# Performance work log

Hardware: AMD Instinct MI355X
Metric: run time of the kernel (lower is better)

Reference implementation:

```python
import jax, jax.numpy as jnp
import numpy as np

EPS = 1e-6

def setup_inputs() -> dict:
    key = jax.random.key(0)
    ks = jax.random.split(key, 7)
    T, B, S, A, D = 512, 32, 64, 8, 32
    x = jax.random.normal(ks[0], (T, B, D), dtype=jnp.float32)
    a = jax.random.normal(ks[1], (T, B, A), dtype=jnp.float32)
    mask = jnp.ones((T, B), dtype=jnp.float32)
    mu = jax.random.normal(ks[2], (S, D), dtype=jnp.float32)
    logv = 0.1 * jax.random.normal(ks[3], (S, D), dtype=jnp.float32)
    init_logits = jax.random.normal(ks[4], (S,), dtype=jnp.float32)
    w_base = 0.1 * jax.random.normal(ks[5], (S, S), dtype=jnp.float32)
    w_act = 0.1 * jax.random.normal(ks[6], (A, S, S), dtype=jnp.float32)
    return {"x": x, "a": a, "mask": mask, "mu": mu, "logv": logv,
            "init_logits": init_logits, "w_base": w_base, "w_act": w_act}

def reference(x, a, mask, mu, logv, init_logits, w_base, w_act):
    T, B, D = x.shape
    S = mu.shape[0]
    # Gaussian (diag) emission log-likelihood for every state: [T, B, S]
    var = jnp.exp(logv)
    diff = x[:, :, None, :] - mu  # [T, B, S, D]
    logp_x = -0.5 * jnp.sum(diff * diff / var + logv + jnp.log(2.0 * jnp.pi), axis=-1)
    # Logistic (action-conditioned) transition matrices for t=1..T-1: [T-1, B, S, S]
    trans = jax.nn.softmax(w_base + jnp.einsum('tba,aij->tbij', a[:-1], w_act), axis=-1)
    logp0 = jax.nn.log_softmax(init_logits)
    # alpha_0
    alpha0 = jax.nn.softmax(logp_x[0] + logp0, axis=-1)

    def fwd_step(b, inp):
        tr, lx = inp
        logp_z = jnp.log(jnp.sum(tr * b[:, :, None] + EPS, axis=-2))
        b_new = jax.nn.softmax(lx + logp_z, axis=-1)
        return b_new, b_new

    _, alpha_rest = jax.lax.scan(fwd_step, alpha0, (trans, logp_x[1:]))
    alpha = jnp.concatenate([alpha0[None], alpha_rest], axis=0)  # [T, B, S]

    log_trans = jnp.log(trans + EPS)

    def bwd_step(logb, inp):
        ltr, lx, m = inp
        new = jax.scipy.special.logsumexp(lx[:, None, :] + ltr + logb[:, None, :], axis=-1)
        new = new * (m[:, None] == 1)
        return new, new

    _, lb = jax.lax.scan(bwd_step, jnp.zeros((B, S), x.dtype),
                         (log_trans, logp_x[1:], mask[1:]), reverse=True)
    log_beta = jnp.concatenate([lb, jnp.zeros((1, B, S), x.dtype)], axis=0)  # [T, B, S]

    # Posterior state marginals
    q_z = jax.nn.softmax(jnp.log(alpha + EPS) + log_beta, axis=-1)
    return q_z
```

## Files before the change

### kernel.cpp

```cpp
#include <hip/hip_runtime.h>
#include <math.h>

#define TT 512
#define BB 32
#define SS 64
#define AA 8
#define DD 32
#define EPSF 1e-6f
#define SEPS (64.0f * 1e-6f)
#define TS 68

__device__ __forceinline__ int   f2i(float x){ return __float_as_int(x); }
__device__ __forceinline__ float i2f(int x){ return __int_as_float(x); }
__device__ __forceinline__ float readlane_f(float v, int l){
  return i2f(__builtin_amdgcn_readlane(f2i(v), l));
}
template<int CTRL, int RMASK>
__device__ __forceinline__ float dpp_add(float x){
  return x + i2f(__builtin_amdgcn_update_dpp(0, f2i(x), CTRL, RMASK, 0xf, true));
}
__device__ __forceinline__ float wave_sum_dpp(float x){
  x = dpp_add<0x111, 0xf>(x);
  x = dpp_add<0x112, 0xf>(x);
  x = dpp_add<0x114, 0xf>(x);
  x = dpp_add<0x118, 0xf>(x);
  x = dpp_add<0x142, 0xa>(x);
  x = dpp_add<0x143, 0xc>(x);
  return readlane_f(x, 63);
}
__device__ __forceinline__ float wave_sum(float v){
  #pragma unroll
  for (int m = 1; m < 64; m <<= 1) v += __shfl_xor(v, m, 64);
  return v;
}
__device__ __forceinline__ float wave_max(float v){
  #pragma unroll
  for (int m = 1; m < 64; m <<= 1) v = fmaxf(v, __shfl_xor(v, m, 64));
  return v;
}
#define BARRIER() asm volatile("s_waitcnt lgkmcnt(0)\n\ts_barrier" ::: "memory")

__global__ void prep_kernel(const float* __restrict__ logv,
                            float* __restrict__ iv, float* __restrict__ cs){
  int gid = blockIdx.x * blockDim.x + threadIdx.x;
  if (gid < SS * DD) iv[gid] = __expf(-logv[gid]);
  if (gid < SS){
    float s = 0.f;
    #pragma unroll
    for (int d = 0; d < DD; ++d) s += logv[gid * DD + d];
    cs[gid] = s + (float)DD * 1.8378770664093453f;
  }
}

__global__ __launch_bounds__(256) void logpx_kernel(
    const float* __restrict__ x, const float* __restrict__ mu,
    const float* __restrict__ iv, const float* __restrict__ cs,
    float* __restrict__ slx_out){
  const int lane = threadIdx.x & 63;
  const int w = threadIdx.x >> 6;
  const int row = blockIdx.x * 4 + w;
  const float* __restrict__ xp  = x  + row * DD;
  const float* __restrict__ mup = mu + lane * DD;
  const float* __restrict__ ivp = iv + lane * DD;
  float acc = 0.f;
  #pragma unroll
  for (int d = 0; d < DD; ++d){
    float diff = xp[d] - mup[d];
    acc = fmaf(diff * diff, ivp[d], acc);
  }
  float lx = -0.5f * (acc + cs[lane]);
  float mx = wave_max(lx);
  slx_out[row * SS + lane] = lx - mx;
}

__global__ __launch_bounds__(768) void scan_kernel(
    const float* __restrict__ slx, const float* __restrict__ mask,
    const float* __restrict__ il, const float* __restrict__ a,
    const float* __restrict__ w_base, const float* __restrict__ w_act,
    float* __restrict__ alpha, float* __restrict__ log_beta){
  const int lane = threadIdx.x & 63;
  const int w    = threadIdx.x >> 6;
  const bool is_fwd = (blockIdx.x < BB);
  const int b = is_fwd ? blockIdx.x : (blockIdx.x - BB);

  __shared__ __align__(16) float tile[3][SS * TS];
  __shared__ float rsp[3][8][SS];
  __shared__ float fpart[2][4][SS];
  __shared__ __align__(16) float aLDS[TT * AA];
  __shared__ float mLDS[TT];

  for (int idx = threadIdx.x; idx < TT * AA; idx += 768){
    int t = idx >> 3, k = idx & 7;
    aLDS[idx] = a[(t * BB + b) * AA + k];
  }
  for (int idx = threadIdx.x; idx < TT; idx += 768)
    mLDS[idx] = mask[idx * BB + b];

  if (w >= 4){
    const int pw = w - 4;
    const int jb = pw * 8;
    float wb[8], wa[8][8];
    #pragma unroll
    for (int jj = 0; jj < 8; ++jj){
      wb[jj] = w_base[lane * SS + jb + jj];
      #pragma unroll
      for (int k = 0; k < 8; ++k)
        wa[k][jj] = w_act[(k * SS + lane) * SS + jb + jj];
    }
    float aa[8], aan[8];
    {
      const int t0 = is_fwd ? 0 : (TT - 2);
      const float* __restrict__ ap = a + (t0 * BB + b) * AA;
      #pragma unroll
      for (int k = 0; k < 8; ++k) aa[k] = ap[k];
      const int t1 = is_fwd ? 1 : (TT - 3);
      const float* __restrict__ ap1 = a + (t1 * BB + b) * AA;
      #pragma unroll
      for (int k = 0; k < 8; ++k) aan[k] = ap1[k];
    }
    {
      float ev[8]; float racc = 0.f;
      #pragma unroll
      for (int jj = 0; jj < 8; ++jj){
        float u = wb[jj];
        #pragma unroll
        for (int k = 0; k < 8; ++k) u = fmaf(aa[k], wa[k][jj], u);
        ev[jj] = __expf(u); racc += ev[jj];
      }
      *(float4*)&tile[0][lane * TS + jb]     = make_float4(ev[0],ev[1],ev[2],ev[3]);
      *(float4*)&tile[0][lane * TS + jb + 4] = make_float4(ev[4],ev[5],ev[6],ev[7]);
      rsp[0][pw][lane] = racc;
    }
    BARRIER();
    int tw = 1;
    for (int s = 0; s < TT - 1; ++s){
      if (s <= TT - 3){
        #pragma unroll
        for (int k = 0; k < 8; ++k) aa[k] = aan[k];
        if (s + 1 <= TT - 3){
          const int tn = is_fwd ? (s + 2) : (TT - 4 - s);
          #pragma unroll
          for (int k = 0; k < 8; ++k) aan[k] = aLDS[tn * AA + k];
        }
        float ev[8]; float racc = 0.f;
        #pragma unroll
        for (int jj = 0; jj < 8; ++jj){
          float u = wb[jj];
          #pragma unroll
          for (int k = 0; k < 8; ++k) u = fmaf(aa[k], wa[k][jj], u);
          ev[jj] = __expf(u); racc += ev[jj];
        }
        *(float4*)&tile[tw][lane * TS + jb]     = make_float4(ev[0],ev[1],ev[2],ev[3]);
        *(float4*)&tile[tw][lane * TS + jb + 4] = make_float4(ev[4],ev[5],ev[6],ev[7]);
        rsp[tw][pw][lane] = racc;
        tw = (tw == 2) ? 0 : tw + 1;
      }
      BARRIER();
    }
  } else if (is_fwd){
    const int wb16 = __builtin_amdgcn_readfirstlane(w * 16);
    float u = __expf(slx[b * SS + lane] + il[lane]);
    float c = __builtin_amdgcn_rcpf(wave_sum_dpp(u));
    if (w == 0) alpha[b * SS + lane] = u * c;
    float slxn = slx[(BB + b) * SS + lane];
    float elxc = 0.f;
    BARRIER();
    int ts = 0;
    for (int s = 0; s < TT - 1; ++s){
      if (s > 0){
        const int fs = (s - 1) & 1;
        float S = (fpart[fs][0][lane] + fpart[fs][1][lane])
                + (fpart[fs][2][lane] + fpart[fs][3][lane]);
        u = elxc * fmaf(c, S, SEPS);
        c = __builtin_amdgcn_rcpf(wave_sum_dpp(u));
        if (w == 0) alpha[(s * BB + b) * SS + lane] = u * c;
      }
      float rs = ((rsp[ts][0][lane] + rsp[ts][1][lane]) + (rsp[ts][2][lane] + rsp[ts][3][lane]))
               + ((rsp[ts][4][lane] + rsp[ts][5][lane]) + (rsp[ts][6][lane] + rsp[ts][7][lane]));
      float va = u * __builtin_amdgcn_rcpf(rs);
      const float* __restrict__ tp = &tile[ts][0];
      float a0 = 0.f, a1 = 0.f, a2 = 0.f, a3 = 0.f;
      #pragma unroll
      for (int r = 0; r < 16; r += 4){
        a0 = fmaf(readlane_f(va, wb16 + r    ), tp[(wb16 + r    ) * TS + lane], a0);
        a1 = fmaf(readlane_f(va, wb16 + r + 1), tp[(wb16 + r + 1) * TS + lane], a1);
        a2 = fmaf(readlane_f(va, wb16 + r + 2), tp[(wb16 + r + 2) * TS + lane], a2);
        a3 = fmaf(readlane_f(va, wb16 + r + 3), tp[(wb16 + r + 3) * TS + lane], a3);
      }
      fpart[s & 1][w][lane] = (a0 + a1) + (a2 + a3);
      elxc = __expf(slxn);
      if (s + 2 <= TT - 1) slxn = slx[((s + 2) * BB + b) * SS + lane];
      ts = (ts == 2) ? 0 : ts + 1;
      BARRIER();
    }
    {
      const int fs = (TT - 2) & 1;
      float S = (fpart[fs][0][lane] + fpart[fs][1][lane])
              + (fpart[fs][2][lane] + fpart[fs][3][lane]);
      u = elxc * fmaf(c, S, SEPS);
      c = __builtin_amdgcn_rcpf(wave_sum_dpp(u));
      if (w == 0) alpha[((TT - 1) * BB + b) * SS + lane] = u * c;
    }
  } else {
    const int wb16 = __builtin_amdgcn_readfirstlane(w * 16);
    float breg = 0.f, rWc = 1.f;
    if (w == 0) log_beta[((TT - 1) * BB + b) * SS + lane] = 0.f;
    float slxc = slx[((TT - 1) * BB + b) * SS + lane];
    float mprev = 1.f;
    BARRIER();
    int ts = 0, pts = 2;
    for (int s = 0; s < TT - 1; ++s){
      if (s > 0){
        const int fs = (s - 1) & 1;
        float eh = (fpart[fs][0][lane] + fpart[fs][1][lane])
                 + (fpart[fs][2][lane] + fpart[fs][3][lane]);
        float rsv = ((rsp[pts][0][lane] + rsp[pts][1][lane]) + (rsp[pts][2][lane] + rsp[pts][3][lane]))
                  + ((rsp[pts][4][lane] + rsp[pts][5][lane]) + (rsp[pts][6][lane] + rsp[pts][7][lane]));
        float v = __logf(fmaf(eh * __builtin_amdgcn_rcpf(rsv), rWc, EPSF));
        breg = (mprev == 1.0f) ? v : 0.0f;
        if (w == 0) log_beta[((TT - 1 - s) * BB + b) * SS + lane] = breg;
      }
      float wgt = __expf(slxc + breg);
      float W = wave_sum_dpp(wgt);
      rWc = __builtin_amdgcn_rcpf(W);
      const float* __restrict__ tp = &tile[ts][lane * TS + wb16];
      float4 e0 = *(const float4*)(tp);
      float4 e1 = *(const float4*)(tp + 4);
      float4 e2 = *(const float4*)(tp + 8);
      float4 e3 = *(const float4*)(tp + 12);
      float a0 = 0.f, a1 = 0.f, a2 = 0.f, a3 = 0.f;
      a0 = fmaf(readlane_f(wgt, wb16 + 0),  e0.x, a0);
      a1 = fmaf(readlane_f(wgt, wb16 + 1),  e0.y, a1);
      a2 = fmaf(readlane_f(wgt, wb16 + 2),  e0.z, a2);
      a3 = fmaf(readlane_f(wgt, wb16 + 3),  e0.w, a3);
      a0 = fmaf(readlane_f(wgt, wb16 + 4),  e1.x, a0);
      a1 = fmaf(readlane_f(wgt, wb16 + 5),  e1.y, a1);
      a2 = fmaf(readlane_f(wgt, wb16 + 6),  e1.z, a2);
      a3 = fmaf(readlane_f(wgt, wb16 + 7),  e1.w, a3);
      a0 = fmaf(readlane_f(wgt, wb16 + 8),  e2.x, a0);
      a1 = fmaf(readlane_f(wgt, wb16 + 9),  e2.y, a1);
      a2 = fmaf(readlane_f(wgt, wb16 + 10), e2.z, a2);
      a3 = fmaf(readlane_f(wgt, wb16 + 11), e2.w, a3);
      a0 = fmaf(readlane_f(wgt, wb16 + 12), e3.x, a0);
      a1 = fmaf(readlane_f(wgt, wb16 + 13), e3.y, a1);
      a2 = fmaf(readlane_f(wgt, wb16 + 14), e3.z, a2);
      a3 = fmaf(readlane_f(wgt, wb16 + 15), e3.w, a3);
      fpart[s & 1][w][lane] = (a0 + a1) + (a2 + a3);
      mprev = mLDS[TT - 1 - s];
      if (s <= TT - 3) slxc = slx[((TT - 2 - s) * BB + b) * SS + lane];
      pts = ts; ts = (ts == 2) ? 0 : ts + 1;
      BARRIER();
    }
    {
      const int fs = (TT - 2) & 1;
      float eh = (fpart[fs][0][lane] + fpart[fs][1][lane])
               + (fpart[fs][2][lane] + fpart[fs][3][lane]);
      float rsv = ((rsp[pts][0][lane] + rsp[pts][1][lane]) + (rsp[pts][2][lane] + rsp[pts][3][lane]))
                + ((rsp[pts][4][lane] + rsp[pts][5][lane]) + (rsp[pts][6][lane] + rsp[pts][7][lane]));
      float v = __logf(fmaf(eh * __builtin_amdgcn_rcpf(rsv), rWc, EPSF));
      breg = (mprev == 1.0f) ? v : 0.0f;
      if (w == 0) log_beta[b * SS + lane] = breg;
    }
  }
}

__global__ __launch_bounds__(256) void qz_kernel(
    const float* __restrict__ alpha, const float* __restrict__ log_beta,
    float* __restrict__ out){
  const int lane = threadIdx.x & 63;
  const int w = threadIdx.x >> 6;
  const int row = blockIdx.x * 4 + w;
  float v = __logf(alpha[row * SS + lane] + EPSF) + log_beta[row * SS + lane];
  float mx = wave_max(v);
  float e = __expf(v - mx);
  float sm = wave_sum(e);
  out[row * SS + lane] = e * __builtin_amdgcn_rcpf(sm);
}

extern "C" void kernel_launch(void* const* d_in, const int* in_sizes, int n_in,
                              void* d_out, int out_size, void* d_ws, size_t ws_size,
                              hipStream_t stream){
  const float* x      = (const float*)d_in[0];
  const float* a      = (const float*)d_in[1];
  const float* mask   = (const float*)d_in[2];
  const float* mu     = (const float*)d_in[3];
  const float* logv   = (const float*)d_in[4];
  const float* il     = (const float*)d_in[5];
  const float* w_base = (const float*)d_in[6];
  const float* w_act  = (const float*)d_in[7];
  float* out = (float*)d_out;

  float* ws = (float*)d_ws;
  const size_t TBS = (size_t)TT * BB * SS;
  float* iv       = ws;
  float* cs       = ws + 2048;
  float* slx      = ws + 4096;
  float* alpha    = slx + TBS;
  float* log_beta = alpha + TBS;

  prep_kernel<<<8, 256, 0, stream>>>(logv, iv, cs);
  logpx_kernel<<<TT * BB / 4, 256, 0, stream>>>(x, mu, iv, cs, slx);
  scan_kernel<<<2 * BB, 768, 0, stream>>>(slx, mask, il, a, w_base, w_act,
                                          alpha, log_beta);
  qz_kernel<<<TT * BB / 4, 256, 0, stream>>>(alpha, log_beta, out);
}
```

Measured before the change: 402.4 us.

## Precompute transition softmax in a parallel kernel and stream it into the scan

Adds a fully parallel kernel that computes all action-conditioned transition softmax matrices and writes them to workspace. A new scan kernel then streams those tiles from global memory into a triple-buffered LDS ring, with prefetch waves, instead of recomputing the softmax inside the serial scan. This removes exp/softmax work from the latency-bound recurrence at the cost of writing and reading about 268 MB of extra memory. The new path runs only when the workspace is large enough, otherwise it falls back to the old kernel.

```diff
diff --git a/kernel.cpp b/kernel.cpp
--- a/kernel.cpp
+++ b/kernel.cpp
@@ -71,6 +71,215 @@
   float lx = -0.5f * (acc + cs[lane]);
   float mx = wave_max(lx);
   slx_out[row * SS + lane] = lx - mx;
+}
+
+__global__ __launch_bounds__(512) void trans_kernel(
+    const float* __restrict__ a, const float* __restrict__ w_base,
+    const float* __restrict__ w_act, float* __restrict__ trans){
+  const int b  = blockIdx.x >> 4;
+  const int tc = blockIdx.x & 15;
+  const int t0 = tc * 32;
+  const int tid = threadIdx.x;
+  const int i  = tid >> 3;
+  const int j0 = (tid & 7) * 8;
+  __shared__ float aS[32 * 8];
+  if (tid < 256)
+    aS[tid] = a[(((t0 + (tid >> 3)) * BB) + b) * AA + (tid & 7)];
+  float wb[8], wa[8][8];
+  #pragma unroll
+  for (int jj = 0; jj < 8; ++jj){
+    wb[jj] = w_base[i * SS + j0 + jj];
+    #pragma unroll
+    for (int k = 0; k < 8; ++k)
+      wa[k][jj] = w_act[(k * SS + i) * SS + j0 + jj];
+  }
+  __syncthreads();
+  const int nt = ((TT - 1) - t0 < 32) ? ((TT - 1) - t0) : 32;
+  for (int tt = 0; tt < nt; ++tt){
+    float aa[8];
+    #pragma unroll
+    for (int k = 0; k < 8; ++k) aa[k] = aS[tt * 8 + k];
+    float ev[8]; float rs = 0.f;
+    #pragma unroll
+    for (int jj = 0; jj < 8; ++jj){
+      float u = wb[jj];
+      #pragma unroll
+      for (int k = 0; k < 8; ++k) u = fmaf(aa[k], wa[k][jj], u);
+      ev[jj] = __expf(u); rs += ev[jj];
+    }
+    rs += __shfl_xor(rs, 1, 64);
+    rs += __shfl_xor(rs, 2, 64);
+    rs += __shfl_xor(rs, 4, 64);
+    float rinv = __builtin_amdgcn_rcpf(rs);
+    float* __restrict__ op = trans + ((size_t)(t0 + tt) * BB + b) * (SS * SS)
+                           + i * SS + j0;
+    *(float4*)op       = make_float4(ev[0]*rinv, ev[1]*rinv, ev[2]*rinv, ev[3]*rinv);
+    *(float4*)(op + 4) = make_float4(ev[4]*rinv, ev[5]*rinv, ev[6]*rinv, ev[7]*rinv);
+  }
+}
+
+__global__ __launch_bounds__(512) void scan_pre_kernel(
+    const float* __restrict__ slx, const float* __restrict__ mask,
+    const float* __restrict__ il, const float* __restrict__ trans,
+    float* __restrict__ alpha, float* __restrict__ log_beta){
+  const int lane = threadIdx.x & 63;
+  const int w    = threadIdx.x >> 6;
+  const bool is_fwd = (blockIdx.x < BB);
+  const int b = is_fwd ? blockIdx.x : (blockIdx.x - BB);
+
+  __shared__ __align__(16) float tile[3][SS * TS];
+  __shared__ float fpart[2][4][SS];
+  __shared__ float mLDS[TT];
+
+  for (int idx = threadIdx.x; idx < TT; idx += 512)
+    mLDS[idx] = mask[idx * BB + b];
+
+  if (w >= 4){
+    const int pw = w - 4;
+    const size_t thofs  = (size_t)pw * 1024 + (size_t)lane * 16;
+    const int    ldsoff = (pw * 16 + (lane >> 2)) * TS + (lane & 3) * 16;
+    const size_t tstride = (size_t)BB * SS * SS;
+    const float* gb = trans + (size_t)b * (SS * SS) + thofs;
+    const long gstep = is_fwd ? (long)tstride : -(long)tstride;
+    const float* g0 = is_fwd ? gb : (gb + (size_t)(TT - 2) * tstride);
+    float4 A0,A1,A2,A3, B0,B1,B2,B3;
+    {
+      const float4* gp = (const float4*)g0;
+      float4 c0 = gp[0], c1 = gp[1], c2 = gp[2], c3 = gp[3];
+      const float4* ga = (const float4*)(g0 + gstep);
+      A0 = ga[0]; A1 = ga[1]; A2 = ga[2]; A3 = ga[3];
+      const float4* gbp = (const float4*)(g0 + 2 * gstep);
+      B0 = gbp[0]; B1 = gbp[1]; B2 = gbp[2]; B3 = gbp[3];
+      float* tp = &tile[0][ldsoff];
+      *(float4*)tp = c0; *(float4*)(tp+4) = c1;
+      *(float4*)(tp+8) = c2; *(float4*)(tp+12) = c3;
+    }
+    const float* gcur = g0 + 3 * gstep;
+    BARRIER();
+    int tw = 1;
+    for (int s = 0; s < TT - 1; ++s){
+      if (s <= TT - 3){
+        float* tp = &tile[tw][ldsoff];
+        if ((s & 1) == 0){
+          *(float4*)tp = A0; *(float4*)(tp+4) = A1;
+          *(float4*)(tp+8) = A2; *(float4*)(tp+12) = A3;
+          if (s <= TT - 5){
+            const float4* gp = (const float4*)gcur;
+            A0 = gp[0]; A1 = gp[1]; A2 = gp[2]; A3 = gp[3];
+            gcur += gstep;
+          }
+        } else {
+          *(float4*)tp = B0; *(float4*)(tp+4) = B1;
+          *(float4*)(tp+8) = B2; *(float4*)(tp+12) = B3;
+          if (s <= TT - 5){
+            const float4* gp = (const float4*)gcur;
+            B0 = gp[0]; B1 = gp[1]; B2 = gp[2]; B3 = gp[3];
+            gcur += gstep;
+          }
+        }
+        tw = (tw == 2) ? 0 : tw + 1;
+      }
+      BARRIER();
+    }
+  } else if (is_fwd){
+    const int wb16 = __builtin_amdgcn_readfirstlane(w * 16);
+    float u = __expf(slx[b * SS + lane] + il[lane]);
+    float c = __builtin_amdgcn_rcpf(wave_sum_dpp(u));
+    if (w == 0) alpha[b * SS + lane] = u * c;
+    float slxn = slx[(BB + b) * SS + lane];
+    float elxc = 0.f;
+    BARRIER();
+    int ts = 0;
+    for (int s = 0; s < TT - 1; ++s){
+      if (s > 0){
+        const int fs = (s - 1) & 1;
+        float S = (fpart[fs][0][lane] + fpart[fs][1][lane])
+                + (fpart[fs][2][lane] + fpart[fs][3][lane]);
+        u = elxc * fmaf(c, S, SEPS);
+        c = __builtin_amdgcn_rcpf(wave_sum_dpp(u));
+        if (w == 0) alpha[(s * BB + b) * SS + lane] = u * c;
+      }
+      float va = u;
+      const float* __restrict__ tp = &tile[ts][0];
+      float a0 = 0.f, a1 = 0.f, a2 = 0.f, a3 = 0.f;
+      #pragma unroll
+      for (int r = 0; r < 16; r += 4){
+        a0 = fmaf(readlane_f(va, wb16 + r    ), tp[(wb16 + r    ) * TS + lane], a0);
+        a1 = fmaf(readlane_f(va, wb16 + r + 1), tp[(wb16 + r + 1) * TS + lane], a1);
+        a2 = fmaf(readlane_f(va, wb16 + r + 2), tp[(wb16 + r + 2) * TS + lane], a2);
+        a3 = fmaf(readlane_f(va, wb16 + r + 3), tp[(wb16 + r + 3) * TS + lane], a3);
+      }
+      fpart[s & 1][w][lane] = (a0 + a1) + (a2 + a3);
+      elxc = __expf(slxn);
+      if (s + 2 <= TT - 1) slxn = slx[((s + 2) * BB + b) * SS + lane];
+      ts = (ts == 2) ? 0 : ts + 1;
+      BARRIER();
+    }
+    {
+      const int fs = (TT - 2) & 1;
+      float S = (fpart[fs][0][lane] + fpart[fs][1][lane])
+              + (fpart[fs][2][lane] + fpart[fs][3][lane]);
+      u = elxc * fmaf(c, S, SEPS);
+      c = __builtin_amdgcn_rcpf(wave_sum_dpp(u));
+      if (w == 0) alpha[((TT - 1) * BB + b) * SS + lane] = u * c;
+    }
+  } else {
+    const int wb16 = __builtin_amdgcn_readfirstlane(w * 16);
+    float breg = 0.f, rWc = 1.f;
+    if (w == 0) log_beta[((TT - 1) * BB + b) * SS + lane] = 0.f;
+    float slxc = slx[((TT - 1) * BB + b) * SS + lane];
+    float mprev = 1.f;
+    BARRIER();
+    int ts = 0;
+    for (int s = 0; s < TT - 1; ++s){
+      if (s > 0){
+        const int fs = (s - 1) & 1;
+        float eh = (fpart[fs][0][lane] + fpart[fs][1][lane])
+                 + (fpart[fs][2][lane] + fpart[fs][3][lane]);
+        float v = __logf(fmaf(eh, rWc, EPSF));
+        breg = (mprev == 1.0f) ? v : 0.0f;
+        if (w == 0) log_beta[((TT - 1 - s) * BB + b) * SS + lane] = breg;
+      }
+      float wgt = __expf(slxc + breg);
+      float W = wave_sum_dpp(wgt);
+      rWc = __builtin_amdgcn_rcpf(W);
+      const float* __restrict__ tp = &tile[ts][lane * TS + wb16];
+      float4 e0 = *(const float4*)(tp);
+      float4 e1 = *(const float4*)(tp + 4);
+      float4 e2 = *(const float4*)(tp + 8);
+      float4 e3 = *(const float4*)(tp + 12);
+      float a0 = 0.f, a1 = 0.f, a2 = 0.f, a3 = 0.f;
+      a0 = fmaf(readlane_f(wgt, wb16 + 0),  e0.x, a0);
+      a1 = fmaf(readlane_f(wgt, wb16 + 1),  e0.y, a1);
+      a2 = fmaf(readlane_f(wgt, wb16 + 2),  e0.z, a2);
+      a3 = fmaf(readlane_f(wgt, wb16 + 3),  e0.w, a3);
+      a0 = fmaf(readlane_f(wgt, wb16 + 4),  e1.x, a0);
+      a1 = fmaf(readlane_f(wgt, wb16 + 5),  e1.y, a1);
+      a2 = fmaf(readlane_f(wgt, wb16 + 6),  e1.z, a2);
+      a3 = fmaf(readlane_f(wgt, wb16 + 7),  e1.w, a3);
+      a0 = fmaf(readlane_f(wgt, wb16 + 8),  e2.x, a0);
+      a1 = fmaf(readlane_f(wgt, wb16 + 9),  e2.y, a1);
+      a2 = fmaf(readlane_f(wgt, wb16 + 10), e2.z, a2);
+      a3 = fmaf(readlane_f(wgt, wb16 + 11), e2.w, a3);
+      a0 = fmaf(readlane_f(wgt, wb16 + 12), e3.x, a0);
+      a1 = fmaf(readlane_f(wgt, wb16 + 13), e3.y, a1);
+      a2 = fmaf(readlane_f(wgt, wb16 + 14), e3.z, a2);
+      a3 = fmaf(readlane_f(wgt, wb16 + 15), e3.w, a3);
+      fpart[s & 1][w][lane] = (a0 + a1) + (a2 + a3);
+      mprev = mLDS[TT - 1 - s];
+      if (s <= TT - 3) slxc = slx[((TT - 2 - s) * BB + b) * SS + lane];
+      ts = (ts == 2) ? 0 : ts + 1;
+      BARRIER();
+    }
+    {
+      const int fs = (TT - 2) & 1;
+      float eh = (fpart[fs][0][lane] + fpart[fs][1][lane])
+               + (fpart[fs][2][lane] + fpart[fs][3][lane]);
+      float v = __logf(fmaf(eh, rWc, EPSF));
+      breg = (mprev == 1.0f) ? v : 0.0f;
+      if (w == 0) log_beta[b * SS + lane] = breg;
+    }
+  }
 }
 
 __global__ __launch_bounds__(768) void scan_kernel(
@@ -297,10 +506,20 @@
   float* slx      = ws + 4096;
   float* alpha    = slx + TBS;
   float* log_beta = alpha + TBS;
+  float* trans    = log_beta + TBS;
+
+  const size_t TRANS_FLOATS = (size_t)(TT - 1) * BB * SS * SS;
+  const size_t need_bytes = ((size_t)4096 + 3 * TBS + TRANS_FLOATS) * sizeof(float);
 
   prep_kernel<<<8, 256, 0, stream>>>(logv, iv, cs);
   logpx_kernel<<<TT * BB / 4, 256, 0, stream>>>(x, mu, iv, cs, slx);
-  scan_kernel<<<2 * BB, 768, 0, stream>>>(slx, mask, il, a, w_base, w_act,
-                                          alpha, log_beta);
+  if (ws_size >= need_bytes){
+    trans_kernel<<<512, 512, 0, stream>>>(a, w_base, w_act, trans);
+    scan_pre_kernel<<<2 * BB, 512, 0, stream>>>(slx, mask, il, trans,
+                                                alpha, log_beta);
+  } else {
+    scan_kernel<<<2 * BB, 768, 0, stream>>>(slx, mask, il, a, w_base, w_act,
+                                            alpha, log_beta);
+  }
   qz_kernel<<<TT * BB / 4, 256, 0, stream>>>(alpha, log_beta, out);
 }
```

After: 403.2 us. About the same (+0.2%).

## Precompute transition matrices in a parallel kernel and stream them into the scan

Applied to the files above, without the earlier changes.

Adds a massively parallel kernel that computes the normalized softmax transition matrices for as many timesteps as workspace allows. The producer waves in the scan kernel then stream these precomputed tiles from global memory through a three-deep register prefetch instead of recomputing the exp/FMA work on the serial critical path, falling back to on-the-fly generation for the remaining timesteps. This trades per-step compute in 64 blocks for large global memory traffic (up to 256 MB of writes and reads) and an extra kernel launch.

```diff
diff --git a/kernel.cpp b/kernel.cpp
--- a/kernel.cpp
+++ b/kernel.cpp
@@ -73,10 +73,81 @@
   slx_out[row * SS + lane] = lx - mx;
 }
 
-__global__ __launch_bounds__(768) void scan_kernel(
+__global__ __launch_bounds__(512) void trans_kernel(
+    const float* __restrict__ a, const float* __restrict__ w_base,
+    const float* __restrict__ w_act, float* __restrict__ trans, int F){
+  const int b  = blockIdx.x >> 4;
+  const int tc = blockIdx.x & 15;
+  const int t0 = tc * 32;
+  const int tid = threadIdx.x;
+  const int i  = tid >> 3;
+  const int j0 = (tid & 7) * 8;
+  __shared__ float aS[32 * 8];
+  if (tid < 256)
+    aS[tid] = a[(((t0 + (tid >> 3)) * BB) + b) * AA + (tid & 7)];
+  float wb[8], wa[8][8];
+  #pragma unroll
+  for (int jj = 0; jj < 8; ++jj){
+    wb[jj] = w_base[i * SS + j0 + jj];
+    #pragma unroll
+    for (int k = 0; k < 8; ++k)
+      wa[k][jj] = w_act[(k * SS + i) * SS + j0 + jj];
+  }
+  __syncthreads();
+  int rem = F - t0;
+  const int nt = (rem < 0) ? 0 : (rem < 32 ? rem : 32);
+  for (int tt = 0; tt < nt; ++tt){
+    float aa[8];
+    #pragma unroll
+    for (int k = 0; k < 8; ++k) aa[k] = aS[tt * 8 + k];
+    float ev[8]; float rs = 0.f;
+    #pragma unroll
+    for (int jj = 0; jj < 8; ++jj){
+      float u = wb[jj];
+      #pragma unroll
+      for (int k = 0; k < 8; ++k) u = fmaf(aa[k], wa[k][jj], u);
+      ev[jj] = __expf(u); rs += ev[jj];
+    }
+    rs += __shfl_xor(rs, 1, 64);
+    rs += __shfl_xor(rs, 2, 64);
+    rs += __shfl_xor(rs, 4, 64);
+    float rinv = __builtin_amdgcn_rcpf(rs);
+    float* __restrict__ op = trans + ((size_t)(t0 + tt) * BB + b) * (SS * SS)
+                           + i * SS + j0;
+    *(float4*)op       = make_float4(ev[0]*rinv, ev[1]*rinv, ev[2]*rinv, ev[3]*rinv);
+    *(float4*)(op + 4) = make_float4(ev[4]*rinv, ev[5]*rinv, ev[6]*rinv, ev[7]*rinv);
+  }
+}
+
+#define LOADW() do{ \
+  _Pragma("unroll") \
+  for (int jj = 0; jj < 8; ++jj){ \
+    wb[jj] = w_base[lane * SS + jb + jj]; \
+    _Pragma("unroll") \
+    for (int k = 0; k < 8; ++k) \
+      wa[k][jj] = w_act[(k * SS + lane) * SS + jb + jj]; \
+  } \
+}while(0)
+
+#define GENT(SLOT) do{ \
+  float ev[8]; float racc = 0.f; \
+  _Pragma("unroll") \
+  for (int jj = 0; jj < 8; ++jj){ \
+    float u = wb[jj]; \
+    _Pragma("unroll") \
+    for (int k = 0; k < 8; ++k) u = fmaf(aa[k], wa[k][jj], u); \
+    ev[jj] = __expf(u); racc += ev[jj]; \
+  } \
+  *(float4*)&tile[SLOT][lane * TS + jb]     = make_float4(ev[0],ev[1],ev[2],ev[3]); \
+  *(float4*)&tile[SLOT][lane * TS + jb + 4] = make_float4(ev[4],ev[5],ev[6],ev[7]); \
+  rsp[SLOT][pw][lane] = racc; \
+}while(0)
+
+__global__ __launch_bounds__(768) void scan_hybrid_kernel(
     const float* __restrict__ slx, const float* __restrict__ mask,
     const float* __restrict__ il, const float* __restrict__ a,
     const float* __restrict__ w_base, const float* __restrict__ w_act,
+    const float* __restrict__ trans, int F,
     float* __restrict__ alpha, float* __restrict__ log_beta){
   const int lane = threadIdx.x & 63;
   const int w    = threadIdx.x >> 6;
@@ -99,64 +170,119 @@
   if (w >= 4){
     const int pw = w - 4;
     const int jb = pw * 8;
+    const int g      = pw * 512 + lane * 8;
+    const int ldsoff = (g >> 6) * TS + (g & 63);
+    const size_t tstride = (size_t)BB * SS * SS;
+    const float* __restrict__ gb = trans + (size_t)b * (SS * SS) + g;
+
     float wb[8], wa[8][8];
-    #pragma unroll
-    for (int jj = 0; jj < 8; ++jj){
-      wb[jj] = w_base[lane * SS + jb + jj];
-      #pragma unroll
-      for (int k = 0; k < 8; ++k)
-        wa[k][jj] = w_act[(k * SS + lane) * SS + jb + jj];
-    }
     float aa[8], aan[8];
-    {
-      const int t0 = is_fwd ? 0 : (TT - 2);
-      const float* __restrict__ ap = a + (t0 * BB + b) * AA;
+    const int t0 = is_fwd ? 0 : (TT - 2);
+
+    if (t0 >= F){
+      LOADW();
+      const float* __restrict__ ap = a + ((size_t)t0 * BB + b) * AA;
       #pragma unroll
       for (int k = 0; k < 8; ++k) aa[k] = ap[k];
-      const int t1 = is_fwd ? 1 : (TT - 3);
-      const float* __restrict__ ap1 = a + (t1 * BB + b) * AA;
-      #pragma unroll
-      for (int k = 0; k < 8; ++k) aan[k] = ap1[k];
-    }
-    {
-      float ev[8]; float racc = 0.f;
-      #pragma unroll
-      for (int jj = 0; jj < 8; ++jj){
-        float u = wb[jj];
+      GENT(0);
+    } else {
+      const float4* gp = (const float4*)(gb + (size_t)t0 * tstride);
+      float4 c0 = gp[0], c1 = gp[1];
+      float* tp = &tile[0][ldsoff];
+      *(float4*)tp = c0; *(float4*)(tp + 4) = c1;
+      rsp[0][pw][lane] = 0.125f;
+    }
+    BARRIER();
+    int tw = 1, s = 0;
+
+    if (is_fwd){
+      if (F >= 2){
+        float4 A0, A1, B0, B1, C0, C1;
+        { const float4* p = (const float4*)(gb + 1 * tstride); A0 = p[0]; A1 = p[1]; }
+        if (F >= 3){ const float4* p = (const float4*)(gb + 2 * tstride); B0 = p[0]; B1 = p[1]; }
+        if (F >= 4){ const float4* p = (const float4*)(gb + 3 * tstride); C0 = p[0]; C1 = p[1]; }
+        int tnext = 4, par = 0;
+        for (int ti = 1; ti <= F - 1; ++ti, ++s){
+          float* tp = &tile[tw][ldsoff];
+          if (par == 0){
+            *(float4*)tp = A0; *(float4*)(tp + 4) = A1;
+            if (tnext <= F - 1){ const float4* p = (const float4*)(gb + (size_t)tnext * tstride); A0 = p[0]; A1 = p[1]; ++tnext; }
+          } else if (par == 1){
+            *(float4*)tp = B0; *(float4*)(tp + 4) = B1;
+            if (tnext <= F - 1){ const float4* p = (const float4*)(gb + (size_t)tnext * tstride); B0 = p[0]; B1 = p[1]; ++tnext; }
+          } else {
+            *(float4*)tp = C0; *(float4*)(tp + 4) = C1;
+            if (tnext <= F - 1){ const float4* p = (const float4*)(gb + (size_t)tnext * tstride); C0 = p[0]; C1 = p[1]; ++tnext; }
+          }
+          par = (par == 2) ? 0 : par + 1;
+          rsp[tw][pw][lane] = 0.125f;
+          tw = (tw == 2) ? 0 : tw + 1;
+          BARRIER();
+        }
+      }
+      if (s <= TT - 3){
+        if (t0 < F) LOADW();
+        const int tg0 = s + 1;
         #pragma unroll
-        for (int k = 0; k < 8; ++k) u = fmaf(aa[k], wa[k][jj], u);
-        ev[jj] = __expf(u); racc += ev[jj];
-      }
-      *(float4*)&tile[0][lane * TS + jb]     = make_float4(ev[0],ev[1],ev[2],ev[3]);
-      *(float4*)&tile[0][lane * TS + jb + 4] = make_float4(ev[4],ev[5],ev[6],ev[7]);
-      rsp[0][pw][lane] = racc;
-    }
-    BARRIER();
-    int tw = 1;
-    for (int s = 0; s < TT - 1; ++s){
+        for (int k = 0; k < 8; ++k) aa[k] = aLDS[tg0 * AA + k];
+        for (; s <= TT - 3; ++s){
+          const int tgi = s + 1;
+          if (tgi + 1 <= TT - 2){
+            #pragma unroll
+            for (int k = 0; k < 8; ++k) aan[k] = aLDS[(tgi + 1) * AA + k];
+          }
+          GENT(tw);
+          #pragma unroll
+          for (int k = 0; k < 8; ++k) aa[k] = aan[k];
+          tw = (tw == 2) ? 0 : tw + 1;
+          BARRIER();
+        }
+      }
+    } else {
+      if (s <= TT - 3 && (TT - 3 - s) >= F){
+        const int tg0 = TT - 3;
+        #pragma unroll
+        for (int k = 0; k < 8; ++k) aa[k] = aLDS[tg0 * AA + k];
+        for (; s <= TT - 3 && (TT - 3 - s) >= F; ++s){
+          const int tgi = TT - 3 - s;
+          if (tgi > F){
+            #pragma unroll
+            for (int k = 0; k < 8; ++k) aan[k] = aLDS[(tgi - 1) * AA + k];
+          }
+          GENT(tw);
+          #pragma unroll
+          for (int k = 0; k < 8; ++k) aa[k] = aan[k];
+          tw = (tw == 2) ? 0 : tw + 1;
+          BARRIER();
+        }
+      }
       if (s <= TT - 3){
-        #pragma unroll
-        for (int k = 0; k < 8; ++k) aa[k] = aan[k];
-        if (s + 1 <= TT - 3){
-          const int tn = is_fwd ? (s + 2) : (TT - 4 - s);
-          #pragma unroll
-          for (int k = 0; k < 8; ++k) aan[k] = aLDS[tn * AA + k];
+        const int tc0 = TT - 3 - s;
+        float4 A0, A1, B0, B1, C0, C1;
+        { const float4* p = (const float4*)(gb + (size_t)tc0 * tstride); A0 = p[0]; A1 = p[1]; }
+        if (tc0 - 1 >= 0){ const float4* p = (const float4*)(gb + (size_t)(tc0 - 1) * tstride); B0 = p[0]; B1 = p[1]; }
+        if (tc0 - 2 >= 0){ const float4* p = (const float4*)(gb + (size_t)(tc0 - 2) * tstride); C0 = p[0]; C1 = p[1]; }
+        int tnext = tc0 - 3, par = 0;
+        for (; s <= TT - 3; ++s){
+          float* tp = &tile[tw][ldsoff];
+          if (par == 0){
+            *(float4*)tp = A0; *(float4*)(tp + 4) = A1;
+            if (tnext >= 0){ const float4* p = (const float4*)(gb + (size_t)tnext * tstride); A0 = p[0]; A1 = p[1]; --tnext; }
+          } else if (par == 1){
+            *(float4*)tp = B0; *(float4*)(tp + 4) = B1;
+            if (tnext >= 0){ const float4* p = (const float4*)(gb + (size_t)tnext * tstride); B0 = p[0]; B1 = p[1]; --tnext; }
+          } else {
+            *(float4*)tp = C0; *(float4*)(tp + 4) = C1;
+            if (tnext >= 0){ const float4* p = (const float4*)(gb + (size_t)tnext * tstride); C0 = p[0]; C1 = p[1]; --tnext; }
+          }
+          par = (par == 2) ? 0 : par + 1;
+          rsp[tw][pw][lane] = 0.125f;
+          tw = (tw == 2) ? 0 : tw + 1;
+          BARRIER();
         }
-        float ev[8]; float racc = 0.f;
-        #pragma unroll
-        for (int jj = 0; jj < 8; ++jj){
-          float u = wb[jj];
-          #pragma unroll
-          for (int k = 0; k < 8; ++k) u = fmaf(aa[k], wa[k][jj], u);
-          ev[jj] = __expf(u); racc += ev[jj];
-        }
-        *(float4*)&tile[tw][lane * TS + jb]     = make_float4(ev[0],ev[1],ev[2],ev[3]);
-        *(float4*)&tile[tw][lane * TS + jb + 4] = make_float4(ev[4],ev[5],ev[6],ev[7]);
-        rsp[tw][pw][lane] = racc;
-        tw = (tw == 2) ? 0 : tw + 1;
-      }
-      BARRIER();
-    }
+      }
+    }
+    for (; s <= TT - 2; ++s) BARRIER();
   } else if (is_fwd){
     const int wb16 = __builtin_amdgcn_readfirstlane(w * 16);
     float u = __expf(slx[b * SS + lane] + il[lane]);
@@ -297,10 +423,23 @@
   float* slx      = ws + 4096;
   float* alpha    = slx + TBS;
   float* log_beta = alpha + TBS;
+  float* trans    = log_beta + TBS;
+
+  const long long base_floats = 4096 + 3 * (long long)TBS;
+  const long long tile_floats = (long long)BB * SS * SS;
+  long long availf = (long long)(ws_size / 4) - base_floats;
+  int F = 0;
+  if (availf > 0){
+    long long f = availf / tile_floats;
+    F = (f > (TT - 1)) ? (TT - 1) : (int)f;
+  }
+  if (F < 8) F = 0;
 
   prep_kernel<<<8, 256, 0, stream>>>(logv, iv, cs);
   logpx_kernel<<<TT * BB / 4, 256, 0, stream>>>(x, mu, iv, cs, slx);
-  scan_kernel<<<2 * BB, 768, 0, stream>>>(slx, mask, il, a, w_base, w_act,
-                                          alpha, log_beta);
+  if (F > 0)
+    trans_kernel<<<512, 512, 0, stream>>>(a, w_base, w_act, trans, F);
+  scan_hybrid_kernel<<<2 * BB, 768, 0, stream>>>(slx, mask, il, a, w_base, w_act,
+                                                 trans, F, alpha, log_beta);
   qz_kernel<<<TT * BB / 4, 256, 0, stream>>>(alpha, log_beta, out);
 }
```

New measurement: 505.9 us. 25.7% more time.

## Precompute fp16 transition matrices and run single-wave fp16-dot forward/backward scans

Applied to the files above, without the earlier changes.

Adds a parallel kernel that computes all softmax transition matrices up front and stores them in fp16 in the workspace. Two new single-wave-per-batch scan kernels then stream these matrices from global memory, using packed fp16 dot products with readlane broadcasts and triple-buffered prefetching. This takes the per-step transition computation and block-wide barriers off the sequential critical path. The cost is about 268 MB of extra global traffic and fp16 rounding error. The path is only taken when the workspace is large enough; otherwise the old scan kernel runs.

```diff
diff --git a/kernel.cpp b/kernel.cpp
--- a/kernel.cpp
+++ b/kernel.cpp
@@ -1,4 +1,5 @@
 #include <hip/hip_runtime.h>
+#include <hip/hip_fp16.h>
 #include <math.h>
 
 #define TT 512
@@ -10,10 +11,19 @@
 #define SEPS (64.0f * 1e-6f)
 #define TS 68
 
+typedef _Float16 h2_t __attribute__((ext_vector_type(2)));
+typedef __fp16   fp16v2 __attribute__((ext_vector_type(2)));
+
 __device__ __forceinline__ int   f2i(float x){ return __float_as_int(x); }
 __device__ __forceinline__ float i2f(int x){ return __int_as_float(x); }
 __device__ __forceinline__ float readlane_f(float v, int l){
   return i2f(__builtin_amdgcn_readlane(f2i(v), l));
+}
+__device__ __forceinline__ h2_t i2h2(int x){ return __builtin_bit_cast(h2_t, x); }
+__device__ __forceinline__ h2_t u2h2(unsigned x){ return __builtin_bit_cast(h2_t, x); }
+__device__ __forceinline__ int pkrtz_i(float a, float b){
+  fp16v2 p = __builtin_amdgcn_cvt_pkrtz(a, b);
+  return __builtin_bit_cast(int, p);
 }
 template<int CTRL, int RMASK>
 __device__ __forceinline__ float dpp_add(float x){
@@ -28,6 +38,9 @@
   x = dpp_add<0x143, 0xc>(x);
   return readlane_f(x, 63);
 }
+__device__ __forceinline__ float dpp_xor1(float x){
+  return i2f(__builtin_amdgcn_update_dpp(0, f2i(x), 0xB1, 0xf, 0xf, true));
+}
 __device__ __forceinline__ float wave_sum(float v){
   #pragma unroll
   for (int m = 1; m < 64; m <<= 1) v += __shfl_xor(v, m, 64);
@@ -39,6 +52,20 @@
   return v;
 }
 #define BARRIER() asm volatile("s_waitcnt lgkmcnt(0)\n\ts_barrier" ::: "memory")
+
+__device__ __forceinline__ unsigned pk2(float a, float b){
+  return (unsigned)__half_as_ushort(__float2half_rn(a))
+       | ((unsigned)__half_as_ushort(__float2half_rn(b)) << 16);
+}
+
+#if __has_builtin(__builtin_amdgcn_fdot2)
+#define FDOT2(A, B, C) __builtin_amdgcn_fdot2((A), (B), (C), false)
+#else
+__device__ __forceinline__ float fdot2_emul(h2_t a, h2_t b, float c){
+  return fmaf((float)a.x, (float)b.x, fmaf((float)a.y, (float)b.y, c));
+}
+#define FDOT2(A, B, C) fdot2_emul((A), (B), (C))
+#endif
 
 __global__ void prep_kernel(const float* __restrict__ logv,
                             float* __restrict__ iv, float* __restrict__ cs){
@@ -71,6 +98,151 @@
   float lx = -0.5f * (acc + cs[lane]);
   float mx = wave_max(lx);
   slx_out[row * SS + lane] = lx - mx;
+}
+
+__global__ __launch_bounds__(512) void trans_kernel(
+    const float* __restrict__ a, const float* __restrict__ w_base,
+    const float* __restrict__ w_act, unsigned short* __restrict__ trans, int F){
+  const int b  = blockIdx.x >> 4;
+  const int tc = blockIdx.x & 15;
+  const int t0 = tc * 32;
+  const int q    = threadIdx.x >> 6;
+  const int j    = threadIdx.x & 63;
+  __shared__ float aS[32 * 8];
+  if (threadIdx.x < 256)
+    aS[threadIdx.x] = a[(((t0 + (threadIdx.x >> 3)) * BB) + b) * AA + (threadIdx.x & 7)];
+  float wb[8], wa[8][8];
+  #pragma unroll
+  for (int e = 0; e < 8; ++e){
+    wb[e] = w_base[(8 * q + e) * SS + j];
+    #pragma unroll
+    for (int k = 0; k < 8; ++k)
+      wa[k][e] = w_act[(k * SS + 8 * q + e) * SS + j];
+  }
+  __syncthreads();
+  int rem = F - t0;
+  const int nt = (rem < 0) ? 0 : (rem < 32 ? rem : 32);
+  for (int tt = 0; tt < nt; ++tt){
+    float aa[8];
+    #pragma unroll
+    for (int k = 0; k < 8; ++k) aa[k] = aS[tt * 8 + k];
+    float ev[8], rs[8];
+    #pragma unroll
+    for (int e = 0; e < 8; ++e){
+      float u = wb[e];
+      #pragma unroll
+      for (int k = 0; k < 8; ++k) u = fmaf(aa[k], wa[k][e], u);
+      ev[e] = __expf(u); rs[e] = ev[e];
+    }
+    #pragma unroll
+    for (int m = 1; m < 64; m <<= 1){
+      #pragma unroll
+      for (int e = 0; e < 8; ++e) rs[e] += __shfl_xor(rs[e], m, 64);
+    }
+    float ri[8];
+    #pragma unroll
+    for (int e = 0; e < 8; ++e) ri[e] = __builtin_amdgcn_rcpf(rs[e]);
+    uint4 o;
+    o.x = pk2(ev[0] * ri[0], ev[1] * ri[1]);
+    o.y = pk2(ev[2] * ri[2], ev[3] * ri[3]);
+    o.z = pk2(ev[4] * ri[4], ev[5] * ri[5]);
+    o.w = pk2(ev[6] * ri[6], ev[7] * ri[7]);
+    *(uint4*)(trans + ((size_t)(t0 + tt) * BB + b) * (SS * SS) + q * 512 + j * 8) = o;
+  }
+}
+
+__global__ __launch_bounds__(64) void scan_wave_kernel(
+    const float* __restrict__ slx, const float* __restrict__ mask,
+    const float* __restrict__ il, const unsigned short* __restrict__ trans,
+    float* __restrict__ alpha, float* __restrict__ log_beta){
+  const int lane = threadIdx.x;
+  const bool is_fwd = (blockIdx.x < BB);
+  const int b = is_fwd ? blockIdx.x : (blockIdx.x - BB);
+
+  if (is_fwd){
+    uint4 A[8], B[8], C[8];
+#define LOADT(ARR, t) do{ \
+    const uint4* p_ = (const uint4*)(trans + ((size_t)(t) * BB + b) * (SS * SS) + lane * 8); \
+    _Pragma("unroll") \
+    for (int q_ = 0; q_ < 8; ++q_) ARR[q_] = p_[q_ * 64]; \
+  }while(0)
+#define DOTQ(ARR, Q) \
+    a0 = FDOT2(i2h2(__builtin_amdgcn_readlane(upki, 8*Q + 0)), u2h2(ARR[Q].x), a0); \
+    a1 = FDOT2(i2h2(__builtin_amdgcn_readlane(upki, 8*Q + 2)), u2h2(ARR[Q].y), a1); \
+    a2 = FDOT2(i2h2(__builtin_amdgcn_readlane(upki, 8*Q + 4)), u2h2(ARR[Q].z), a2); \
+    a3 = FDOT2(i2h2(__builtin_amdgcn_readlane(upki, 8*Q + 6)), u2h2(ARR[Q].w), a3);
+#define DOTS(ARR) \
+    DOTQ(ARR,0) DOTQ(ARR,1) DOTQ(ARR,2) DOTQ(ARR,3) \
+    DOTQ(ARR,4) DOTQ(ARR,5) DOTQ(ARR,6) DOTQ(ARR,7)
+
+    LOADT(A, 0); LOADT(B, 1); LOADT(C, 2);
+    float u = __expf(slx[b * SS + lane] + il[lane]);
+    float c = __builtin_amdgcn_rcpf(wave_sum_dpp(u));
+    alpha[b * SS + lane] = u * c;
+    float slxn = slx[(BB + b) * SS + lane];
+    int par = 0;
+    for (int s = 0; s <= TT - 2; ++s){
+      float elxc = __expf(slxn);
+      if (s + 2 <= TT - 1) slxn = slx[((s + 2) * BB + b) * SS + lane];
+      float usw = dpp_xor1(u);
+      int upki = pkrtz_i(u, usw);
+      float a0 = 0.f, a1 = 0.f, a2 = 0.f, a3 = 0.f;
+      if (par == 0){
+        DOTS(A); if (s + 3 <= TT - 2) LOADT(A, s + 3);
+      } else if (par == 1){
+        DOTS(B); if (s + 3 <= TT - 2) LOADT(B, s + 3);
+      } else {
+        DOTS(C); if (s + 3 <= TT - 2) LOADT(C, s + 3);
+      }
+      par = (par == 2) ? 0 : par + 1;
+      float S = (a0 + a1) + (a2 + a3);
+      u = elxc * fmaf(c, S, SEPS);
+      c = __builtin_amdgcn_rcpf(wave_sum_dpp(u));
+      alpha[((s + 1) * BB + b) * SS + lane] = u * c;
+    }
+  } else {
+    int r[64];
+#define LOADR(t) do{ \
+    const unsigned short* pb_ = trans + ((size_t)(t) * BB + b) * (SS * SS) \
+                              + (lane >> 3) * 512 + (lane & 7); \
+    _Pragma("unroll") \
+    for (int j_ = 0; j_ < 64; ++j_) r[j_] = pb_[j_ * 8]; \
+  }while(0)
+
+    LOADR(TT - 2);
+    float breg = 0.f;
+    log_beta[((TT - 1) * BB + b) * SS + lane] = 0.f;
+    float slxc = slx[((TT - 1) * BB + b) * SS + lane];
+    float mg = mask[(TT - 1) * BB + b];
+    for (int s = 0; s <= TT - 2; ++s){
+      const int t = TT - 2 - s;
+      int hh[32];
+      #pragma unroll
+      for (int m = 0; m < 32; ++m) hh[m] = r[2 * m] | (r[2 * m + 1] << 16);
+      if (s + 1 <= TT - 2) LOADR(t - 1);
+      float wgt = __expf(slxc + breg);
+      float W = wave_sum_dpp(wgt);
+      float rW = __builtin_amdgcn_rcpf(W);
+      float wsw = dpp_xor1(wgt);
+      int wpki = pkrtz_i(wgt, wsw);
+      float a0 = 0.f, a1 = 0.f, a2 = 0.f, a3 = 0.f;
+      #pragma unroll
+      for (int m = 0; m < 32; m += 4){
+        a0 = FDOT2(i2h2(__builtin_amdgcn_readlane(wpki, 2*m + 0)), i2h2(hh[m + 0]), a0);
+        a1 = FDOT2(i2h2(__builtin_amdgcn_readlane(wpki, 2*m + 2)), i2h2(hh[m + 1]), a1);
+        a2 = FDOT2(i2h2(__builtin_amdgcn_readlane(wpki, 2*m + 4)), i2h2(hh[m + 2]), a2);
+        a3 = FDOT2(i2h2(__builtin_amdgcn_readlane(wpki, 2*m + 6)), i2h2(hh[m + 3]), a3);
+      }
+      float S = (a0 + a1) + (a2 + a3);
+      float v = __logf(fmaf(S, rW, EPSF));
+      breg = (mg == 1.0f) ? v : 0.0f;
+      log_beta[(t * BB + b) * SS + lane] = breg;
+      if (s + 1 <= TT - 2){
+        slxc = slx[(t * BB + b) * SS + lane];
+        mg = mask[t * BB + b];
+      }
+    }
+  }
 }
 
 __global__ __launch_bounds__(768) void scan_kernel(
@@ -297,10 +469,20 @@
   float* slx      = ws + 4096;
   float* alpha    = slx + TBS;
   float* log_beta = alpha + TBS;
+  unsigned short* trans = (unsigned short*)(log_beta + TBS);
+
+  const size_t base_bytes = ((size_t)4096 + 3 * TBS) * 4;
+  const size_t full_bytes = base_bytes + (size_t)(TT - 1) * BB * SS * SS * 2;
 
   prep_kernel<<<8, 256, 0, stream>>>(logv, iv, cs);
   logpx_kernel<<<TT * BB / 4, 256, 0, stream>>>(x, mu, iv, cs, slx);
-  scan_kernel<<<2 * BB, 768, 0, stream>>>(slx, mask, il, a, w_base, w_act,
-                                          alpha, log_beta);
+  if (ws_size >= full_bytes){
+    trans_kernel<<<512, 512, 0, stream>>>(a, w_base, w_act, trans, TT - 1);
+    scan_wave_kernel<<<2 * BB, 64, 0, stream>>>(slx, mask, il, trans,
+                                                alpha, log_beta);
+  } else {
+    scan_kernel<<<2 * BB, 768, 0, stream>>>(slx, mask, il, a, w_base, w_act,
+                                            alpha, log_beta);
+  }
   qz_kernel<<<TT * BB / 4, 256, 0, stream>>>(alpha, log_beta, out);
 }
```

Result: slower. 561.1 us (+39.5%).
